# Kernel tuning notes

Measured on AMD Instinct MI355X. Metric: run time of the kernel, lower is better.

## Reference

```python
import jax, jax.numpy as jnp
import numpy as np

VIDEO_DIM, TEXT_DIM, ATTN_DIM = 1024, 768, 512
B, S1, S2 = 8, 256, 64


def setup_inputs() -> dict:
    key = jax.random.key(0)
    ks = jax.random.split(key, 10)
    return {
        "video": jax.random.normal(ks[0], (B, S1, VIDEO_DIM), dtype=jnp.float32),
        "text": jax.random.normal(ks[1], (B, S2, TEXT_DIM), dtype=jnp.float32),
        "video_mask": jax.random.randint(ks[2], (B, S1), 0, 2, dtype=jnp.int32),
        "text_mask": jax.random.randint(ks[3], (B, S2), 0, 2, dtype=jnp.int32),
        "w1": jax.random.normal(ks[4], (VIDEO_DIM, ATTN_DIM), dtype=jnp.float32),
        "w2": jax.random.normal(ks[5], (TEXT_DIM, ATTN_DIM), dtype=jnp.float32),
        "w3": jax.random.normal(ks[6], (ATTN_DIM, 1), dtype=jnp.float32),
        "bias": jax.random.normal(ks[7], (ATTN_DIM,), dtype=jnp.float32),
        "w4": jax.random.normal(ks[8], (ATTN_DIM * 4, 500), dtype=jnp.float32),
        "b4": jax.random.normal(ks[9], (500,), dtype=jnp.float32),
    }


def reference(video, text, video_mask, text_mask, w1, w2, w3, bias, w4, b4):
    # NOTE: original torch code calls h.masked_fill(...) (non in-place) and
    # discards the result, so video_mask/text_mask have NO effect. Faithful.
    # Project before broadcasting (mathematically identical to expand-then-matmul).
    h1 = jnp.einsum("bpd,da->bpa", video, w1)   # [b,s1,a]
    h2 = jnp.einsum("bqd,da->bqa", text, w2)    # [b,s2,a]
    # broadcast additive attention: [b,s1,s2,a]
    h = jnp.tanh(h1[:, :, None, :] + h2[:, None, :, :] + bias)
    e = jnp.einsum("bpqa,ao->bpq", h, w3)       # [b,s1,s2] (w3 has out-dim 1)
    # softmax over text dim (dim=2); the expand to attn_dim is uniform, so
    # softmax per-channel equals softmax of the scalar score.
    scores = jax.nn.softmax(e, axis=2)          # [b,s1,s2]
    text_attn = jnp.einsum("bpq,bqa->bpa", scores, h2)  # [b,s1,a]
    hh = h1                                      # video @ w1, same projection
    cont = jnp.concatenate([hh, text_attn, hh * text_attn, hh - text_attn], axis=-1)
    ret = jnp.einsum("bpc,co->bpo", jnp.tanh(cont), w4) + b4
    return ret
```

## Files before the change

### kernel.cpp

```cpp
#include <hip/hip_runtime.h>
#include <hip/hip_bf16.h>
#include <cstddef>

#define MBP   2048
#define MT    512
#define ADIM  512
#define VDIM  1024
#define TDIM  768
#define NOUT  500
#define CDIM  2048

typedef __attribute__((ext_vector_type(8))) short short8;
typedef __attribute__((ext_vector_type(4))) float floatx4;

__device__ __forceinline__ float tanh_fast(float x) {
    float e = __builtin_amdgcn_exp2f(x * 2.88539008177793f);
    float r = __builtin_amdgcn_rcpf(e + 1.0f);
    return __builtin_fmaf(-2.0f, r, 1.0f);
}

__device__ __forceinline__ unsigned short bf16r(float x) {
    union { float f; unsigned int u; } c; c.f = x;
    unsigned int r = (c.u + 0x7fffu + ((c.u >> 16) & 1u)) >> 16;
    return (unsigned short)r;
}
__device__ __forceinline__ float bf2f(unsigned short h) {
    union { unsigned int u; float f; } c; c.u = ((unsigned int)h) << 16;
    return c.f;
}

__global__ __launch_bounds__(256) void conv_split(
    const float* __restrict__ src,
    unsigned short* __restrict__ hi, unsigned short* __restrict__ lo, int n4)
{
    int i = blockIdx.x * 256 + threadIdx.x;
    if (i < n4) {
        float4 v = ((const float4*)src)[i];
        ushort4 h, l;
        h.x = bf16r(v.x); l.x = bf16r(v.x - bf2f(h.x));
        h.y = bf16r(v.y); l.y = bf16r(v.y - bf2f(h.y));
        h.z = bf16r(v.z); l.z = bf16r(v.z - bf2f(h.z));
        h.w = bf16r(v.w); l.w = bf16r(v.w - bf2f(h.w));
        ((ushort4*)hi)[i] = h;
        ((ushort4*)lo)[i] = l;
    }
}

__global__ __launch_bounds__(256) void transp_split(
    const float* __restrict__ src,
    unsigned short* __restrict__ hi, unsigned short* __restrict__ lo, int R, int C)
{
    __shared__ float tile[32][33];
    const float* s = src + (size_t)blockIdx.z * R * C;
    unsigned short* dh = hi + (size_t)blockIdx.z * R * C;
    unsigned short* dl = lo + (size_t)blockIdx.z * R * C;
    const int tx = threadIdx.x & 31, ty = threadIdx.x >> 5;
    const int r0 = blockIdx.x * 32, c0 = blockIdx.y * 32;
    #pragma unroll
    for (int i = 0; i < 4; ++i) {
        int r = r0 + ty + i * 8, c = c0 + tx;
        if (r < R && c < C) tile[ty + i * 8][tx] = s[(size_t)r * C + c];
    }
    __syncthreads();
    #pragma unroll
    for (int i = 0; i < 4; ++i) {
        int c = c0 + ty + i * 8, r = r0 + tx;
        if (c < C && r < R) {
            float v = tile[tx][ty + i * 8];
            unsigned short h = bf16r(v);
            dh[(size_t)c * R + r] = h;
            dl[(size_t)c * R + r] = bf16r(v - bf2f(h));
        }
    }
}

__global__ __launch_bounds__(256) void transp_bf16(
    const float* __restrict__ src, unsigned short* __restrict__ dst, int R, int C)
{
    __shared__ float tile[32][33];
    const int tx = threadIdx.x & 31, ty = threadIdx.x >> 5;
    const int r0 = blockIdx.x * 32, c0 = blockIdx.y * 32;
    #pragma unroll
    for (int i = 0; i < 4; ++i) {
        int r = r0 + ty + i * 8, c = c0 + tx;
        if (r < R && c < C) tile[ty + i * 8][tx] = src[(size_t)r * C + c];
    }
    __syncthreads();
    #pragma unroll
    for (int i = 0; i < 4; ++i) {
        int c = c0 + ty + i * 8, r = r0 + tx;
        if (c < C && r < R) dst[(size_t)c * R + r] = bf16r(tile[tx][ty + i * 8]);
    }
}

#define LP 40

__global__ __launch_bounds__(256) void gemm3_bf16(
    const unsigned short* __restrict__ Ah, const unsigned short* __restrict__ Al,
    const unsigned short* __restrict__ Bh, const unsigned short* __restrict__ Bl,
    float* __restrict__ C, int M, int N, int K)
{
    __shared__ __align__(16) unsigned short Ahs[2][64 * LP];
    __shared__ __align__(16) unsigned short Als[2][64 * LP];
    __shared__ __align__(16) unsigned short Bhs[2][64 * LP];
    __shared__ __align__(16) unsigned short Bls[2][64 * LP];

    const int t = threadIdx.x;
    const int r  = t >> 2;
    const int kc = (t & 3) << 3;
    const int row0 = blockIdx.x * 64, col0 = blockIdx.y * 64;
    const int wave = t >> 6, lane = t & 63;
    const int m15 = lane & 15, q8 = (lane >> 4) << 3;

    const size_t aoff = (size_t)(row0 + r) * K + kc;
    const size_t boff = (size_t)(col0 + r) * K + kc;

    floatx4 acc[4] = { {0.f,0.f,0.f,0.f}, {0.f,0.f,0.f,0.f},
                       {0.f,0.f,0.f,0.f}, {0.f,0.f,0.f,0.f} };

    uint4 avh = *(const uint4*)(Ah + aoff);
    uint4 avl = *(const uint4*)(Al + aoff);
    uint4 bvh = *(const uint4*)(Bh + boff);
    uint4 bvl = *(const uint4*)(Bl + boff);
    *(uint4*)&Ahs[0][r * LP + kc] = avh;
    *(uint4*)&Als[0][r * LP + kc] = avl;
    *(uint4*)&Bhs[0][r * LP + kc] = bvh;
    *(uint4*)&Bls[0][r * LP + kc] = bvl;

    const int nIter = K >> 5;
    for (int i = 0; i < nIter; ++i) {
        __syncthreads();
        if (i + 1 < nIter) {
            int k0 = (i + 1) << 5;
            avh = *(const uint4*)(Ah + aoff + k0);
            avl = *(const uint4*)(Al + aoff + k0);
            bvh = *(const uint4*)(Bh + boff + k0);
            bvl = *(const uint4*)(Bl + boff + k0);
        }
        const int cur = i & 1;
        short8 afh = *(const short8*)&Ahs[cur][(wave * 16 + m15) * LP + q8];
        short8 afl = *(const short8*)&Als[cur][(wave * 16 + m15) * LP + q8];
        #pragma unroll
        for (int j = 0; j < 4; ++j) {
            short8 bfh = *(const short8*)&Bhs[cur][(j * 16 + m15) * LP + q8];
            short8 bfl = *(const short8*)&Bls[cur][(j * 16 + m15) * LP + q8];
            acc[j] = __builtin_amdgcn_mfma_f32_16x16x32_bf16(afh, bfh, acc[j], 0, 0, 0);
            acc[j] = __builtin_amdgcn_mfma_f32_16x16x32_bf16(afh, bfl, acc[j], 0, 0, 0);
            acc[j] = __builtin_amdgcn_mfma_f32_16x16x32_bf16(afl, bfh, acc[j], 0, 0, 0);
        }
        if (i + 1 < nIter) {
            const int nxt = cur ^ 1;
            *(uint4*)&Ahs[nxt][r * LP + kc] = avh;
            *(uint4*)&Als[nxt][r * LP + kc] = avl;
            *(uint4*)&Bhs[nxt][r * LP + kc] = bvh;
            *(uint4*)&Bls[nxt][r * LP + kc] = bvl;
        }
    }

    const int rbase = row0 + wave * 16 + (q8 >> 1);
    #pragma unroll
    for (int j = 0; j < 4; ++j) {
        int col = col0 + j * 16 + m15;
        #pragma unroll
        for (int rr = 0; rr < 4; ++rr)
            C[(size_t)(rbase + rr) * N + col] = acc[j][rr];
    }
}

__global__ __launch_bounds__(256) void gemm_bf16(
    const unsigned short* __restrict__ A, const unsigned short* __restrict__ Bt,
    const float* __restrict__ bias, float* __restrict__ C,
    int M, int N, int K)
{
    __shared__ __align__(16) unsigned short As[2][64 * LP];
    __shared__ __align__(16) unsigned short Bs[2][64 * LP];

    const int t = threadIdx.x;
    const int r  = t >> 2;
    const int kc = (t & 3) << 3;
    const int row0 = blockIdx.x * 64, col0 = blockIdx.y * 64;
    const int wave = t >> 6, lane = t & 63;
    const int m15 = lane & 15, q8 = (lane >> 4) << 3;

    const unsigned short* Ap = A + (size_t)(row0 + r) * K + kc;
    const int bn = col0 + r;
    const unsigned short* Bp = Bt + (size_t)bn * K + kc;
    const bool bvalid = (bn < N);

    floatx4 acc[4] = { {0.f,0.f,0.f,0.f}, {0.f,0.f,0.f,0.f},
                       {0.f,0.f,0.f,0.f}, {0.f,0.f,0.f,0.f} };

    uint4 av = *(const uint4*)Ap;
    uint4 bv = {0u,0u,0u,0u};
    if (bvalid) bv = *(const uint4*)Bp;
    *(uint4*)&As[0][r * LP + kc] = av;
    *(uint4*)&Bs[0][r * LP + kc] = bv;

    const int nIter = K >> 5;
    for (int i = 0; i < nIter; ++i) {
        __syncthreads();
        if (i + 1 < nIter) {
            int k0 = (i + 1) << 5;
            av = *(const uint4*)(Ap + k0);
            if (bvalid) bv = *(const uint4*)(Bp + k0);
        }
        const int cur = i & 1;
        short8 af = *(const short8*)&As[cur][(wave * 16 + m15) * LP + q8];
        #pragma unroll
        for (int j = 0; j < 4; ++j) {
            short8 bf = *(const short8*)&Bs[cur][(j * 16 + m15) * LP + q8];
            acc[j] = __builtin_amdgcn_mfma_f32_16x16x32_bf16(af, bf, acc[j], 0, 0, 0);
        }
        if (i + 1 < nIter) {
            const int nxt = cur ^ 1;
            *(uint4*)&As[nxt][r * LP + kc] = av;
            *(uint4*)&Bs[nxt][r * LP + kc] = bv;
        }
    }

    const int rbase = row0 + wave * 16 + (q8 >> 1);
    #pragma unroll
    for (int j = 0; j < 4; ++j) {
        int col = col0 + j * 16 + m15;
        if (col < N) {
            float bvadd = bias ? bias[col] : 0.0f;
            #pragma unroll
            for (int rr = 0; rr < 4; ++rr)
                C[(size_t)(rbase + rr) * N + col] = acc[j][rr] + bvadd;
        }
    }
}

#define NP 4
#define TA 128
__global__ __launch_bounds__(256) void attn_scores(
    const float* __restrict__ h1,
    const float* __restrict__ h2,
    const float* __restrict__ bias,
    const float* __restrict__ w3,
    unsigned short* __restrict__ sc_h,
    unsigned short* __restrict__ sc_l)
{
    __shared__ __align__(16) float  h2t[TA / 4][64][4];
    __shared__ __align__(16) float2 h1bw[NP][ADIM];

    const int bp0 = blockIdx.x * NP;
    const int b   = bp0 >> 8;
    const int t   = threadIdx.x;
    const int wave = t >> 6, lane = t & 63;
    const float* h2b = h2 + (size_t)b * 64 * ADIM;

    for (int i = t; i < NP * ADIM; i += 256) {
        int p = i >> 9, a = i & 511;
        h1bw[p][a] = make_float2(h1[(size_t)(bp0 + p) * ADIM + a] + bias[a], w3[a]);
    }

    float acc = 0.f;
    for (int tile = 0; tile < ADIM / TA; ++tile) {
        const int a0 = tile * TA;
        __syncthreads();
        #pragma unroll
        for (int i = 0; i < TA / (NP * 4); ++i) {
            int a4 = (wave * (TA / (NP * 4)) + i) * 4;
            float4 v = *(const float4*)(h2b + (size_t)lane * ADIM + a0 + a4);
            *(float4*)&h2t[a4 >> 2][lane][0] = v;
        }
        __syncthreads();
        const float2* bw = &h1bw[wave][a0];
        #pragma unroll 8
        for (int g = 0; g < TA / 4; ++g) {
            float4 hv = *(const float4*)&h2t[g][lane][0];
            float2 c0 = bw[g * 4 + 0], c1 = bw[g * 4 + 1];
            float2 c2 = bw[g * 4 + 2], c3 = bw[g * 4 + 3];
            acc = __builtin_fmaf(tanh_fast(c0.x + hv.x), c0.y, acc);
            acc = __builtin_fmaf(tanh_fast(c1.x + hv.y), c1.y, acc);
            acc = __builtin_fmaf(tanh_fast(c2.x + hv.z), c2.y, acc);
            acc = __builtin_fmaf(tanh_fast(c3.x + hv.w), c3.y, acc);
        }
    }

    float m = acc;
    #pragma unroll
    for (int off = 32; off; off >>= 1) m = fmaxf(m, __shfl_xor(m, off, 64));
    float ex = __builtin_amdgcn_exp2f((acc - m) * 1.44269504088896f);
    float s = ex;
    #pragma unroll
    for (int off = 32; off; off >>= 1) s += __shfl_xor(s, off, 64);
    float sc = ex * __builtin_amdgcn_rcpf(s);
    unsigned short h = bf16r(sc);
    size_t oidx = (size_t)(bp0 + wave) * 64 + lane;
    sc_h[oidx] = h;
    sc_l[oidx] = bf16r(sc - bf2f(h));
}

__global__ __launch_bounds__(256) void ta_cont(
    const unsigned short* __restrict__ sc_h,
    const unsigned short* __restrict__ sc_l,
    const unsigned short* __restrict__ h2t_h,
    const unsigned short* __restrict__ h2t_l,
    const float* __restrict__ h1,
    unsigned short* __restrict__ tcont)
{
    const int row0 = blockIdx.x * 64;
    const int col0 = blockIdx.y * 64;
    const int b = row0 >> 8;
    const int t = threadIdx.x;
    const int wave = t >> 6, lane = t & 63;
    const int m15 = lane & 15, q8 = (lane >> 4) << 3;

    const size_t aidx = (size_t)(row0 + wave * 16 + m15) * 64 + q8;
    short8 af0h = *(const short8*)&sc_h[aidx];
    short8 af1h = *(const short8*)&sc_h[aidx + 32];
    short8 af0l = *(const short8*)&sc_l[aidx];
    short8 af1l = *(const short8*)&sc_l[aidx + 32];
    const size_t bbase = (size_t)b * ADIM * 64;

    floatx4 acc[4];
    #pragma unroll
    for (int j = 0; j < 4; ++j) {
        size_t boff = bbase + (size_t)(col0 + j * 16 + m15) * 64 + q8;
        short8 bf0h = *(const short8*)&h2t_h[boff];
        short8 bf1h = *(const short8*)&h2t_h[boff + 32];
        short8 bf0l = *(const short8*)&h2t_l[boff];
        short8 bf1l = *(const short8*)&h2t_l[boff + 32];
        floatx4 z = {0.f, 0.f, 0.f, 0.f};
        z = __builtin_amdgcn_mfma_f32_16x16x32_bf16(af0h, bf0h, z, 0, 0, 0);
        z = __builtin_amdgcn_mfma_f32_16x16x32_bf16(af0h, bf0l, z, 0, 0, 0);
        z = __builtin_amdgcn_mfma_f32_16x16x32_bf16(af0l, bf0h, z, 0, 0, 0);
        z = __builtin_amdgcn_mfma_f32_16x16x32_bf16(af1h, bf1h, z, 0, 0, 0);
        z = __builtin_amdgcn_mfma_f32_16x16x32_bf16(af1h, bf1l, z, 0, 0, 0);
        acc[j] = __builtin_amdgcn_mfma_f32_16x16x32_bf16(af1l, bf1h, z, 0, 0, 0);
    }

    const int rbase = row0 + wave * 16 + (q8 >> 1);
    #pragma unroll
    for (int j = 0; j < 4; ++j) {
        int a = col0 + j * 16 + m15;
        #pragma unroll
        for (int rr = 0; rr < 4; ++rr) {
            int row = rbase + rr;
            float ta = acc[j][rr];
            float hh = h1[(size_t)row * ADIM + a];
            unsigned short* o = tcont + (size_t)row * CDIM;
            o[a]            = bf16r(tanh_fast(hh));
            o[ADIM + a]     = bf16r(tanh_fast(ta));
            o[2 * ADIM + a] = bf16r(tanh_fast(hh * ta));
            o[3 * ADIM + a] = bf16r(tanh_fast(hh - ta));
        }
    }
}

extern "C" void kernel_launch(void* const* d_in, const int* in_sizes, int n_in,
                              void* d_out, int out_size, void* d_ws, size_t ws_size,
                              hipStream_t stream) {
    const float* video = (const float*)d_in[0];
    const float* text  = (const float*)d_in[1];
    const float* w1   = (const float*)d_in[4];
    const float* w2   = (const float*)d_in[5];
    const float* w3   = (const float*)d_in[6];
    const float* bias = (const float*)d_in[7];
    const float* w4   = (const float*)d_in[8];
    const float* b4   = (const float*)d_in[9];
    float* out = (float*)d_out;

    char* ws = (char*)d_ws;
    size_t off = 0;
    unsigned short* vid_h = (unsigned short*)(ws + off); off += (size_t)MBP * VDIM * 2;
    unsigned short* vid_l = (unsigned short*)(ws + off); off += (size_t)MBP * VDIM * 2;
    unsigned short* txt_h = (unsigned short*)(ws + off); off += (size_t)MT * TDIM * 2;
    unsigned short* txt_l = (unsigned short*)(ws + off); off += (size_t)MT * TDIM * 2;
    unsigned short* w1t_h = (unsigned short*)(ws + off); off += (size_t)ADIM * VDIM * 2;
    unsigned short* w1t_l = (unsigned short*)(ws + off); off += (size_t)ADIM * VDIM * 2;
    unsigned short* w2t_h = (unsigned short*)(ws + off); off += (size_t)ADIM * TDIM * 2;
    unsigned short* w2t_l = (unsigned short*)(ws + off); off += (size_t)ADIM * TDIM * 2;
    unsigned short* w4t   = (unsigned short*)(ws + off); off += (size_t)NOUT * CDIM * 2;
    float*          h1    = (float*)(ws + off);          off += (size_t)MBP * ADIM * 4;
    float*          h2    = (float*)(ws + off);          off += (size_t)MT * ADIM * 4;
    unsigned short* sc_h  = (unsigned short*)(ws + off); off += (size_t)MBP * 64 * 2;
    unsigned short* sc_l  = (unsigned short*)(ws + off); off += (size_t)MBP * 64 * 2;
    unsigned short* h2t_h = (unsigned short*)(ws + off); off += (size_t)8 * ADIM * 64 * 2;
    unsigned short* h2t_l = (unsigned short*)(ws + off); off += (size_t)8 * ADIM * 64 * 2;
    unsigned short* tc    = (unsigned short*)(ws + off); off += (size_t)MBP * CDIM * 2;

    conv_split<<<(MBP * VDIM / 4 + 255) / 256, 256, 0, stream>>>(video, vid_h, vid_l, MBP * VDIM / 4);
    conv_split<<<(MT * TDIM / 4 + 255) / 256, 256, 0, stream>>>(text, txt_h, txt_l, MT * TDIM / 4);
    transp_split<<<dim3(VDIM / 32, ADIM / 32, 1), 256, 0, stream>>>(w1, w1t_h, w1t_l, VDIM, ADIM);
    transp_split<<<dim3(TDIM / 32, ADIM / 32, 1), 256, 0, stream>>>(w2, w2t_h, w2t_l, TDIM, ADIM);
    transp_bf16<<<dim3(CDIM / 32, (NOUT + 31) / 32), 256, 0, stream>>>(w4, w4t, CDIM, NOUT);

    gemm3_bf16<<<dim3(MBP / 64, ADIM / 64), 256, 0, stream>>>(vid_h, vid_l, w1t_h, w1t_l, h1, MBP, ADIM, VDIM);
    gemm3_bf16<<<dim3(MT / 64, ADIM / 64), 256, 0, stream>>>(txt_h, txt_l, w2t_h, w2t_l, h2, MT, ADIM, TDIM);

    transp_split<<<dim3(64 / 32, ADIM / 32, 8), 256, 0, stream>>>(h2, h2t_h, h2t_l, 64, ADIM);

    attn_scores<<<MBP / NP, 256, 0, stream>>>(h1, h2, bias, w3, sc_h, sc_l);

    ta_cont<<<dim3(MBP / 64, ADIM / 64), 256, 0, stream>>>(sc_h, sc_l, h2t_h, h2t_l, h1, tc);

    gemm_bf16<<<dim3(MBP / 64, (NOUT + 63) / 64), 256, 0, stream>>>(tc, w4t, b4, out, MBP, NOUT, CDIM);
}
```

Before: 182.4 us.

## Merge prep conversions into one launch and fuse both projection GEMMs with h2 transpose

Five separate conversion/transpose kernels become a single prep kernel that dispatches on block index. The two split-bf16 projection GEMMs merge into one grid covering both video and text rows, which also removes a launch. The text GEMM epilogue writes the transposed hi/lo bf16 copy of h2 directly, eliminating the separate transpose kernel. This cuts launch overhead and one global round trip. The cost is scattered 2-byte stores in the epilogue and some branch divergence between block types.

```diff
diff --git a/kernel.cpp b/kernel.cpp
--- a/kernel.cpp
+++ b/kernel.cpp
@@ -29,37 +29,32 @@
     return c.f;
 }
 
-__global__ __launch_bounds__(256) void conv_split(
-    const float* __restrict__ src,
-    unsigned short* __restrict__ hi, unsigned short* __restrict__ lo, int n4)
-{
-    int i = blockIdx.x * 256 + threadIdx.x;
-    if (i < n4) {
-        float4 v = ((const float4*)src)[i];
-        ushort4 h, l;
-        h.x = bf16r(v.x); l.x = bf16r(v.x - bf2f(h.x));
-        h.y = bf16r(v.y); l.y = bf16r(v.y - bf2f(h.y));
-        h.z = bf16r(v.z); l.z = bf16r(v.z - bf2f(h.z));
-        h.w = bf16r(v.w); l.w = bf16r(v.w - bf2f(h.w));
-        ((ushort4*)hi)[i] = h;
-        ((ushort4*)lo)[i] = l;
-    }
-}
-
-__global__ __launch_bounds__(256) void transp_split(
-    const float* __restrict__ src,
-    unsigned short* __restrict__ hi, unsigned short* __restrict__ lo, int R, int C)
-{
-    __shared__ float tile[32][33];
-    const float* s = src + (size_t)blockIdx.z * R * C;
-    unsigned short* dh = hi + (size_t)blockIdx.z * R * C;
-    unsigned short* dl = lo + (size_t)blockIdx.z * R * C;
+__device__ __forceinline__ void conv_split_body(
+    const float* __restrict__ src, unsigned short* __restrict__ hi,
+    unsigned short* __restrict__ lo, int blk)
+{
+    int i = blk * 256 + threadIdx.x;
+    float4 v = ((const float4*)src)[i];
+    ushort4 h, l;
+    h.x = bf16r(v.x); l.x = bf16r(v.x - bf2f(h.x));
+    h.y = bf16r(v.y); l.y = bf16r(v.y - bf2f(h.y));
+    h.z = bf16r(v.z); l.z = bf16r(v.z - bf2f(h.z));
+    h.w = bf16r(v.w); l.w = bf16r(v.w - bf2f(h.w));
+    ((ushort4*)hi)[i] = h;
+    ((ushort4*)lo)[i] = l;
+}
+
+__device__ __forceinline__ void transp_split_body(
+    float (*tile)[33], const float* __restrict__ src,
+    unsigned short* __restrict__ hi, unsigned short* __restrict__ lo,
+    int R, int C, int bx, int by)
+{
     const int tx = threadIdx.x & 31, ty = threadIdx.x >> 5;
-    const int r0 = blockIdx.x * 32, c0 = blockIdx.y * 32;
+    const int r0 = bx * 32, c0 = by * 32;
     #pragma unroll
     for (int i = 0; i < 4; ++i) {
         int r = r0 + ty + i * 8, c = c0 + tx;
-        if (r < R && c < C) tile[ty + i * 8][tx] = s[(size_t)r * C + c];
+        if (r < R && c < C) tile[ty + i * 8][tx] = src[(size_t)r * C + c];
     }
     __syncthreads();
     #pragma unroll
@@ -68,18 +63,18 @@
         if (c < C && r < R) {
             float v = tile[tx][ty + i * 8];
             unsigned short h = bf16r(v);
-            dh[(size_t)c * R + r] = h;
-            dl[(size_t)c * R + r] = bf16r(v - bf2f(h));
-        }
-    }
-}
-
-__global__ __launch_bounds__(256) void transp_bf16(
-    const float* __restrict__ src, unsigned short* __restrict__ dst, int R, int C)
-{
-    __shared__ float tile[32][33];
+            hi[(size_t)c * R + r] = h;
+            lo[(size_t)c * R + r] = bf16r(v - bf2f(h));
+        }
+    }
+}
+
+__device__ __forceinline__ void transp_single_body(
+    float (*tile)[33], const float* __restrict__ src,
+    unsigned short* __restrict__ dst, int R, int C, int bx, int by)
+{
     const int tx = threadIdx.x & 31, ty = threadIdx.x >> 5;
-    const int r0 = blockIdx.x * 32, c0 = blockIdx.y * 32;
+    const int r0 = bx * 32, c0 = by * 32;
     #pragma unroll
     for (int i = 0; i < 4; ++i) {
         int r = r0 + ty + i * 8, c = c0 + tx;
@@ -93,22 +88,60 @@
     }
 }
 
+__global__ __launch_bounds__(256) void prep(
+    const float* __restrict__ video, const float* __restrict__ text,
+    const float* __restrict__ w1, const float* __restrict__ w2,
+    const float* __restrict__ w4,
+    unsigned short* __restrict__ vid_h, unsigned short* __restrict__ vid_l,
+    unsigned short* __restrict__ txt_h, unsigned short* __restrict__ txt_l,
+    unsigned short* __restrict__ w1t_h, unsigned short* __restrict__ w1t_l,
+    unsigned short* __restrict__ w2t_h, unsigned short* __restrict__ w2t_l,
+    unsigned short* __restrict__ w4t)
+{
+    __shared__ float tile[32][33];
+    const int bid = blockIdx.x;
+    if (bid < 2048) {
+        conv_split_body(video, vid_h, vid_l, bid);
+    } else if (bid < 2432) {
+        conv_split_body(text, txt_h, txt_l, bid - 2048);
+    } else if (bid < 2944) {
+        int idx = bid - 2432;
+        transp_split_body(tile, w1, w1t_h, w1t_l, VDIM, ADIM, idx & 31, idx >> 5);
+    } else if (bid < 3328) {
+        int idx = bid - 2944;
+        transp_split_body(tile, w2, w2t_h, w2t_l, TDIM, ADIM, idx % 24, idx / 24);
+    } else {
+        int idx = bid - 3328;
+        transp_single_body(tile, w4, w4t, CDIM, NOUT, idx & 63, idx >> 6);
+    }
+}
+
 #define LP 40
 
-__global__ __launch_bounds__(256) void gemm3_bf16(
-    const unsigned short* __restrict__ Ah, const unsigned short* __restrict__ Al,
-    const unsigned short* __restrict__ Bh, const unsigned short* __restrict__ Bl,
-    float* __restrict__ C, int M, int N, int K)
+__global__ __launch_bounds__(256) void gemm3_both(
+    const unsigned short* __restrict__ vid_h, const unsigned short* __restrict__ vid_l,
+    const unsigned short* __restrict__ w1t_h, const unsigned short* __restrict__ w1t_l,
+    const unsigned short* __restrict__ txt_h, const unsigned short* __restrict__ txt_l,
+    const unsigned short* __restrict__ w2t_h, const unsigned short* __restrict__ w2t_l,
+    float* __restrict__ h1, float* __restrict__ h2,
+    unsigned short* __restrict__ h2t_h, unsigned short* __restrict__ h2t_l)
 {
     __shared__ __align__(16) unsigned short Ahs[2][64 * LP];
     __shared__ __align__(16) unsigned short Als[2][64 * LP];
     __shared__ __align__(16) unsigned short Bhs[2][64 * LP];
     __shared__ __align__(16) unsigned short Bls[2][64 * LP];
 
+    const bool isH2 = (blockIdx.x >= 32);
+    const unsigned short *Ah, *Al, *Bh, *Bl;
+    float* C;
+    int K, row0;
+    if (!isH2) { Ah = vid_h; Al = vid_l; Bh = w1t_h; Bl = w1t_l; C = h1; K = VDIM; row0 = blockIdx.x * 64; }
+    else       { Ah = txt_h; Al = txt_l; Bh = w2t_h; Bl = w2t_l; C = h2; K = TDIM; row0 = (blockIdx.x - 32) * 64; }
+
     const int t = threadIdx.x;
     const int r  = t >> 2;
     const int kc = (t & 3) << 3;
-    const int row0 = blockIdx.x * 64, col0 = blockIdx.y * 64;
+    const int col0 = blockIdx.y * 64;
     const int wave = t >> 6, lane = t & 63;
     const int m15 = lane & 15, q8 = (lane >> 4) << 3;
 
@@ -162,8 +195,17 @@
     for (int j = 0; j < 4; ++j) {
         int col = col0 + j * 16 + m15;
         #pragma unroll
-        for (int rr = 0; rr < 4; ++rr)
-            C[(size_t)(rbase + rr) * N + col] = acc[j][rr];
+        for (int rr = 0; rr < 4; ++rr) {
+            int row = rbase + rr;
+            float v = acc[j][rr];
+            C[(size_t)row * ADIM + col] = v;
+            if (isH2) {
+                size_t idx = (size_t)(row >> 6) * (ADIM * 64) + (size_t)col * 64 + (row & 63);
+                unsigned short h = bf16r(v);
+                h2t_h[idx] = h;
+                h2t_l[idx] = bf16r(v - bf2f(h));
+            }
+        }
     }
 }
 
@@ -382,16 +424,13 @@
     unsigned short* h2t_l = (unsigned short*)(ws + off); off += (size_t)8 * ADIM * 64 * 2;
     unsigned short* tc    = (unsigned short*)(ws + off); off += (size_t)MBP * CDIM * 2;
 
-    conv_split<<<(MBP * VDIM / 4 + 255) / 256, 256, 0, stream>>>(video, vid_h, vid_l, MBP * VDIM / 4);
-    conv_split<<<(MT * TDIM / 4 + 255) / 256, 256, 0, stream>>>(text, txt_h, txt_l, MT * TDIM / 4);
-    transp_split<<<dim3(VDIM / 32, ADIM / 32, 1), 256, 0, stream>>>(w1, w1t_h, w1t_l, VDIM, ADIM);
-    transp_split<<<dim3(TDIM / 32, ADIM / 32, 1), 256, 0, stream>>>(w2, w2t_h, w2t_l, TDIM, ADIM);
-    transp_bf16<<<dim3(CDIM / 32, (NOUT + 31) / 32), 256, 0, stream>>>(w4, w4t, CDIM, NOUT);
-
-    gemm3_bf16<<<dim3(MBP / 64, ADIM / 64), 256, 0, stream>>>(vid_h, vid_l, w1t_h, w1t_l, h1, MBP, ADIM, VDIM);
-    gemm3_bf16<<<dim3(MT / 64, ADIM / 64), 256, 0, stream>>>(txt_h, txt_l, w2t_h, w2t_l, h2, MT, ADIM, TDIM);
-
-    transp_split<<<dim3(64 / 32, ADIM / 32, 8), 256, 0, stream>>>(h2, h2t_h, h2t_l, 64, ADIM);
+    prep<<<4352, 256, 0, stream>>>(video, text, w1, w2, w4,
+                                   vid_h, vid_l, txt_h, txt_l,
+                                   w1t_h, w1t_l, w2t_h, w2t_l, w4t);
+
+    gemm3_both<<<dim3(40, 8), 256, 0, stream>>>(vid_h, vid_l, w1t_h, w1t_l,
+                                                txt_h, txt_l, w2t_h, w2t_l,
+                                                h1, h2, h2t_h, h2t_l);
 
     attn_scores<<<MBP / NP, 256, 0, stream>>>(h1, h2, bias, w3, sc_h, sc_l);
 
```

After: 165.1 us. -9.5%, faster.
